# Optimization experiments

Hardware: AMD Instinct MI355X
Metric: run time of the kernel (lower is better)

The kernel has to match this reference:

```python
import jax, jax.numpy as jnp
import numpy as np


def setup_inputs() -> dict:
    key = jax.random.key(0)
    k1, k2 = jax.random.split(key)
    B, S, H, E = 4, 4096, 4096, 64
    hidden_states = jax.random.normal(k1, (B, S, H), dtype=jnp.float32)
    weight = jax.random.normal(k2, (E, H), dtype=jnp.float32) * 0.02
    return {"hidden_states": hidden_states, "weight": weight, "top_k": 8}


def reference(hidden_states, weight, top_k):
    # router logits: (B, S, E) = hidden @ weight.T, computed in fp32 as in torch path
    router_logits = jnp.einsum(
        "bsh,eh->bse",
        hidden_states.astype(jnp.float32),
        weight.astype(jnp.float32),
    )
    topk_weights, topk_indices = jax.lax.top_k(router_logits, top_k)
    topk_weights = jax.nn.softmax(topk_weights, axis=-1)
    return router_logits, topk_indices, topk_weights
```

## Files before the change

kernel.cpp:

```cpp
#include <hip/hip_runtime.h>
#include <math.h>

#define TOKENS 16384
#define HDIM   4096
#define NEXP   64
#define TOPK   8

#define BM 16
#define BK 64
#define CHUNKS (HDIM / BK)

typedef double f64x4 __attribute__((ext_vector_type(4)));

__global__ __launch_bounds__(256) void router_gemm_mfma(const float* __restrict__ hid,
                                                        const float* __restrict__ wgt,
                                                        float* __restrict__ logits) {
    __shared__ float As[2][BM * BK];
    __shared__ float Bs[2][NEXP * BK];

    const int tid  = threadIdx.x;
    const int bm   = blockIdx.x * BM;
    const int wv   = tid >> 6;
    const int lane = tid & 63;
    const int r    = lane & 15;
    const int kq   = lane >> 4;
    const int swz  = r & 7;

    f64x4 rowp = {0., 0., 0., 0.};
    f64x4 colp = {0., 0., 0., 0.};
    rowp = __builtin_amdgcn_mfma_f64_16x16x4f64((double)r, 1.0, rowp, 0, 0, 0);
    colp = __builtin_amdgcn_mfma_f64_16x16x4f64(1.0, (double)r, colp, 0, 0, 0);
    int drow[4], dcol[4];
#pragma unroll
    for (int j = 0; j < 4; ++j) {
        drow[j] = (int)(rowp[j] * 0.25 + 0.5);
        dcol[j] = (int)(colp[j] * 0.25 + 0.5);
    }

    f64x4 acc = {0., 0., 0., 0.};

    const int arow = tid >> 4;
    const int af   = tid & 15;
    const int brow = tid >> 2;
    const int bf   = tid & 3;

    float4 pa, pb[4];

#define LOAD_SET(K0) do { \
        pa = *reinterpret_cast<const float4*>(&hid[(size_t)(bm + arow) * HDIM + (K0) + af * 4]); \
        _Pragma("unroll") \
        for (int j = 0; j < 4; ++j) \
            pb[j] = *reinterpret_cast<const float4*>(&wgt[(size_t)brow * HDIM + (K0) + (bf + 4 * j) * 4]); \
    } while (0)

#define WRITE_SET(BUF) do { \
        *reinterpret_cast<float4*>(&As[BUF][arow * BK + ((af * 4) ^ ((arow & 7) << 2))]) = pa; \
        _Pragma("unroll") \
        for (int j = 0; j < 4; ++j) \
            *reinterpret_cast<float4*>(&Bs[BUF][brow * BK + (((bf + 4 * j) * 4) ^ ((brow & 7) << 2))]) = pb[j]; \
    } while (0)

#define COMPUTE(BUF) do { \
        const float* Ab = &As[BUF][r * BK + kq]; \
        const float* Bb = &Bs[BUF][(wv * 16 + r) * BK + kq]; \
        _Pragma("unroll") \
        for (int ks = 0; ks < 16; ++ks) { \
            const int o = 4 * (ks ^ swz); \
            acc = __builtin_amdgcn_mfma_f64_16x16x4f64((double)Ab[o], (double)Bb[o], acc, 0, 0, 0); \
        } \
    } while (0)

    LOAD_SET(0);
    WRITE_SET(0);

    int cur = 0;
    for (int c = 0; c < CHUNKS; ++c) {
        __syncthreads();
        if (c + 1 < CHUNKS) LOAD_SET((c + 1) * BK);
        COMPUTE(cur);
        if (c + 1 < CHUNKS) WRITE_SET(cur ^ 1);
        cur ^= 1;
    }

#undef LOAD_SET
#undef WRITE_SET
#undef COMPUTE

#pragma unroll
    for (int j = 0; j < 4; ++j) {
        const int row = bm + drow[j];
        const int col = wv * 16 + dcol[j];
        logits[(size_t)row * NEXP + col] = (float)acc[j];
    }
}

__global__ __launch_bounds__(256) void topk_softmax(const float* __restrict__ logits,
                                                    float* __restrict__ out_idx,
                                                    float* __restrict__ out_w) {
    const int wave  = threadIdx.x >> 6;
    const int lane  = threadIdx.x & 63;
    const int token = blockIdx.x * 4 + wave;
    if (token >= TOKENS) return;

    float v = logits[(size_t)token * NEXP + lane];

    float myval = 0.f;
    int   myidx = 0;
    float max0  = 0.f;

#pragma unroll
    for (int k = 0; k < TOPK; ++k) {
        float bv = v;
        int   bi = lane;
#pragma unroll
        for (int off = 32; off > 0; off >>= 1) {
            float ov = __shfl_xor(bv, off);
            int   oi = __shfl_xor(bi, off);
            if (ov > bv || (ov == bv && oi < bi)) { bv = ov; bi = oi; }
        }
        if (k == 0) max0 = bv;
        if (lane == k) { myval = bv; myidx = bi; }
        if (lane == bi) v = -INFINITY;
    }

    float e = (lane < TOPK) ? expf(myval - max0) : 0.f;
    float s = e;
#pragma unroll
    for (int off = 4; off > 0; off >>= 1) s += __shfl_xor(s, off);

    if (lane < TOPK) {
        size_t o = (size_t)token * TOPK + lane;
        out_idx[o] = (float)myidx;
        out_w[o]   = e / s;
    }
}

extern "C" void kernel_launch(void* const* d_in, const int* in_sizes, int n_in,
                              void* d_out, int out_size, void* d_ws, size_t ws_size,
                              hipStream_t stream) {
    const float* hid = (const float*)d_in[0];
    const float* wgt = (const float*)d_in[1];

    float* logits  = (float*)d_out;
    float* out_idx = logits + (size_t)TOKENS * NEXP;
    float* out_w   = out_idx + (size_t)TOKENS * TOPK;

    router_gemm_mfma<<<TOKENS / BM, 256, 0, stream>>>(hid, wgt, logits);
    topk_softmax<<<TOKENS / 4, 256, 0, stream>>>(logits, out_idx, out_w);
}
```

Before: 202.8 us.

## Load GEMM tiles directly into LDS with global_load_lds and split accumulators

Replaces the register-staged global→LDS copy with direct global_load_lds DMA into a unified shared buffer. The tile depth is halved to fit the 16-byte-per-lane segment layout, and the XOR swizzle is moved to the source addresses. The f64 MFMA chain is split into two independent accumulators to shorten the dependency chain. The aim is to remove VGPR staging and LDS write instructions, at the cost of twice as many barriers per K and explicit waitcnt synchronisation.

```diff
diff --git a/kernel.cpp b/kernel.cpp
--- a/kernel.cpp
+++ b/kernel.cpp
@@ -1,5 +1,6 @@
 #include <hip/hip_runtime.h>
 #include <math.h>
+#include <stdint.h>
 
 #define TOKENS 16384
 #define HDIM   4096
@@ -7,7 +8,7 @@
 #define TOPK   8
 
 #define BM 16
-#define BK 64
+#define BK 32
 #define CHUNKS (HDIM / BK)
 
 typedef double f64x4 __attribute__((ext_vector_type(4)));
@@ -15,8 +16,7 @@
 __global__ __launch_bounds__(256) void router_gemm_mfma(const float* __restrict__ hid,
                                                         const float* __restrict__ wgt,
                                                         float* __restrict__ logits) {
-    __shared__ float As[2][BM * BK];
-    __shared__ float Bs[2][NEXP * BK];
+    __shared__ float S[2][2560];
 
     const int tid  = threadIdx.x;
     const int bm   = blockIdx.x * BM;
@@ -37,60 +37,77 @@
         dcol[j] = (int)(colp[j] * 0.25 + 0.5);
     }
 
-    f64x4 acc = {0., 0., 0., 0.};
+    f64x4 acc0 = {0., 0., 0., 0.};
+    f64x4 acc1 = {0., 0., 0., 0.};
 
-    const int arow = tid >> 4;
-    const int af   = tid & 15;
-    const int brow = tid >> 2;
-    const int bf   = tid & 3;
+    const float* segsrc[3];
+    int          segoff[3];
+    int nseg = 0;
+#pragma unroll
+    for (int i = 0; i < 3; ++i) {
+        const int s = wv + 4 * i;
+        if (s < 10) {
+            const int row8 = lane >> 3;
+            if (s < 2) {
+                const int row = s * 8 + row8;
+                const int kg  = (lane & 7) ^ (row & 7);
+                segsrc[i] = hid + (size_t)(bm + row) * HDIM + 4 * kg;
+            } else {
+                const int row = (s - 2) * 8 + row8;
+                const int kg  = (lane & 7) ^ (row & 7);
+                segsrc[i] = wgt + (size_t)row * HDIM + 4 * kg;
+            }
+            segoff[i] = s * 256;
+            nseg = i + 1;
+        }
+    }
 
-    float4 pa, pb[4];
-
-#define LOAD_SET(K0) do { \
-        pa = *reinterpret_cast<const float4*>(&hid[(size_t)(bm + arow) * HDIM + (K0) + af * 4]); \
+#define ISSUE(BUF, K0) do { \
         _Pragma("unroll") \
-        for (int j = 0; j < 4; ++j) \
-            pb[j] = *reinterpret_cast<const float4*>(&wgt[(size_t)brow * HDIM + (K0) + (bf + 4 * j) * 4]); \
-    } while (0)
-
-#define WRITE_SET(BUF) do { \
-        *reinterpret_cast<float4*>(&As[BUF][arow * BK + ((af * 4) ^ ((arow & 7) << 2))]) = pa; \
-        _Pragma("unroll") \
-        for (int j = 0; j < 4; ++j) \
-            *reinterpret_cast<float4*>(&Bs[BUF][brow * BK + (((bf + 4 * j) * 4) ^ ((brow & 7) << 2))]) = pb[j]; \
+        for (int i = 0; i < 3; ++i) { \
+            if (i < nseg) { \
+                const float* src = segsrc[i] + (K0); \
+                __builtin_amdgcn_global_load_lds( \
+                    (const __attribute__((address_space(1))) void*)src, \
+                    (__attribute__((address_space(3))) void*)&S[BUF][segoff[i]], \
+                    16, 0, 0); \
+            } \
+        } \
     } while (0)
 
 #define COMPUTE(BUF) do { \
-        const float* Ab = &As[BUF][r * BK + kq]; \
-        const float* Bb = &Bs[BUF][(wv * 16 + r) * BK + kq]; \
+        const float* Ab = &S[BUF][(r << 5) + kq]; \
+        const float* Bb = &S[BUF][512 + ((wv * 16 + r) << 5) + kq]; \
         _Pragma("unroll") \
-        for (int ks = 0; ks < 16; ++ks) { \
-            const int o = 4 * (ks ^ swz); \
-            acc = __builtin_amdgcn_mfma_f64_16x16x4f64((double)Ab[o], (double)Bb[o], acc, 0, 0, 0); \
+        for (int p = 0; p < 4; ++p) { \
+            const int o0 = 4 * ((2 * p) ^ swz); \
+            const int o1 = 4 * ((2 * p + 1) ^ swz); \
+            acc0 = __builtin_amdgcn_mfma_f64_16x16x4f64((double)Ab[o0], (double)Bb[o0], acc0, 0, 0, 0); \
+            acc1 = __builtin_amdgcn_mfma_f64_16x16x4f64((double)Ab[o1], (double)Bb[o1], acc1, 0, 0, 0); \
         } \
     } while (0)
 
-    LOAD_SET(0);
-    WRITE_SET(0);
+    ISSUE(0, 0);
+    asm volatile("s_waitcnt vmcnt(0)" ::: "memory");
+    __builtin_amdgcn_s_barrier();
 
     int cur = 0;
     for (int c = 0; c < CHUNKS; ++c) {
-        __syncthreads();
-        if (c + 1 < CHUNKS) LOAD_SET((c + 1) * BK);
+        if (c + 1 < CHUNKS) ISSUE(cur ^ 1, (c + 1) * BK);
         COMPUTE(cur);
-        if (c + 1 < CHUNKS) WRITE_SET(cur ^ 1);
+        asm volatile("s_waitcnt vmcnt(0) lgkmcnt(0)" ::: "memory");
+        __builtin_amdgcn_s_barrier();
         cur ^= 1;
     }
 
-#undef LOAD_SET
-#undef WRITE_SET
+#undef ISSUE
 #undef COMPUTE
 
 #pragma unroll
     for (int j = 0; j < 4; ++j) {
         const int row = bm + drow[j];
         const int col = wv * 16 + dcol[j];
-        logits[(size_t)row * NEXP + col] = (float)acc[j];
+        logits[(size_t)row * NEXP + col] = (float)(acc0[j] + acc1[j]);
     }
 }
 
```

New measurement: 224.5 us. 1.11x slower.
